# Optimization experiments

Hardware: AMD Instinct MI355X
Metric: run time of the kernel (lower is better)

## Reference

```python
import jax, jax.numpy as jnp
import numpy as np

SEQ, D_IN, D_OUT = 4096, 1024, 1024

def setup_inputs() -> dict:
    key = jax.random.key(0)
    k1, k2, k3, k4 = jax.random.split(key, 4)
    x = jax.random.normal(k1, (SEQ, D_IN), dtype=jnp.float32)
    # torch Linear weights have shape [d_out, d_in]; y = x @ W.T
    Wq = jax.random.normal(k2, (D_OUT, D_IN), dtype=jnp.float32) * (1.0 / np.sqrt(D_IN))
    Wk = jax.random.normal(k3, (D_OUT, D_IN), dtype=jnp.float32) * (1.0 / np.sqrt(D_IN))
    Wv = jax.random.normal(k4, (D_OUT, D_IN), dtype=jnp.float32) * (1.0 / np.sqrt(D_IN))
    return {"x": x, "Wq": Wq, "Wk": Wk, "Wv": Wv}

def reference(x, Wq, Wk, Wv):
    # q,k,v: [seq, d_out]
    q = x @ Wq.T
    k = x @ Wk.T
    v = x @ Wv.T
    scale = 1.0 / jnp.sqrt(jnp.asarray(k.shape[-1], dtype=x.dtype))
    scores = (q @ k.T) * scale            # [seq, seq]
    attn = jax.nn.softmax(scores, axis=1)  # softmax over key dim (dim=1)
    context = attn @ v                     # [seq, d_out]
    return context
```

## Files before the change

### kernel.cpp

```cpp
#include <hip/hip_runtime.h>

typedef __attribute__((ext_vector_type(4))) float f32x4;
typedef __attribute__((ext_vector_type(8))) short short8;
typedef _Float16 half8 __attribute__((ext_vector_type(8)));

__device__ __forceinline__ unsigned short f2h(float f) {
  _Float16 h = (_Float16)f;
  return __builtin_bit_cast(unsigned short, h);
}
__device__ __forceinline__ float h2f(unsigned short u) {
  return (float)__builtin_bit_cast(_Float16, u);
}

__global__ __launch_bounds__(256) void cast_kernel(const float* __restrict__ in,
                                                   unsigned short* __restrict__ out,
                                                   int n4) {
  int i = blockIdx.x * 256 + threadIdx.x;
  if (i >= n4) return;
  float4 v = ((const float4*)in)[i];
  ushort4 o;
  o.x = f2h(v.x); o.y = f2h(v.y); o.z = f2h(v.z); o.w = f2h(v.w);
  ((ushort4*)out)[i] = o;
}

__global__ __launch_bounds__(256) void cast3_kernel(const float* __restrict__ w0,
                                                    const float* __restrict__ w1,
                                                    const float* __restrict__ w2,
                                                    unsigned short* __restrict__ out) {
  const int b = blockIdx.x;
  const int seg = b >> 10;
  const float* src = (seg == 0) ? w0 : (seg == 1) ? w1 : w2;
  const int i = (b & 1023) * 256 + threadIdx.x;
  float4 v = ((const float4*)src)[i];
  ushort4 o;
  o.x = f2h(v.x); o.y = f2h(v.y); o.z = f2h(v.z); o.w = f2h(v.w);
  ((ushort4*)(out + (size_t)seg * 1048576))[i] = o;
}


#define PHASE(M0, STAGE, TAILWAIT)                                            \
  {                                                                           \
    _Pragma("unroll")                                                         \
    for (int mi = 0; mi < 2; ++mi) {                                          \
      _Pragma("unroll")                                                       \
      for (int ks = 0; ks < 2; ++ks) {                                        \
        const int row = (M0 + mi) * 16 + frow;                                \
        const int e = (row * 64 + ks * 32 + fk) ^ ((row & 7) << 3);           \
        af[mi][ks] = *(const half8*)(const void*)(Acur + e);                  \
      }                                                                       \
    }                                                                         \
    STAGE;                                                                    \
    __builtin_amdgcn_s_barrier();                                             \
    __builtin_amdgcn_s_setprio(1);                                            \
    _Pragma("unroll")                                                         \
    for (int ks = 0; ks < 2; ++ks)                                            \
      _Pragma("unroll")                                                       \
      for (int mi = 0; mi < 2; ++mi)                                          \
        _Pragma("unroll")                                                     \
        for (int n = 0; n < 4; ++n)                                           \
          acc[M0 + mi][n] = __builtin_amdgcn_mfma_f32_16x16x32_f16(           \
              af[mi][ks], bf[n][ks], acc[M0 + mi][n], 0, 0, 0);               \
    __builtin_amdgcn_s_setprio(0);                                            \
    TAILWAIT;                                                                 \
    __builtin_amdgcn_s_barrier();                                             \
  }

template <int MODE>
__global__ __launch_bounds__(512, 2) void gemm8(
    const unsigned short* __restrict__ A, int lda,
    const unsigned short* __restrict__ B, int ldb,
    int ksplit, float alpha,
    float* __restrict__ C0, int ldc0,
    unsigned short* __restrict__ H1, int ldh1,
    unsigned short* __restrict__ H2, int ldh2,
    unsigned short* __restrict__ H3, int ldh3,
    unsigned short* __restrict__ Cqk, int ldqk,
    unsigned short* __restrict__ CvT, int ldvt) {
  __shared__ __attribute__((aligned(16))) unsigned short lds[65536];

  const int t    = threadIdx.x;
  const int lane = t & 63;
  const int wave = t >> 6;
  const int wr   = wave >> 2;
  const int wc   = wave & 3;

  const int nx   = gridDim.x;
  const int nwg  = nx * gridDim.y;
  const int orig = blockIdx.y * nx + blockIdx.x;
  const int wg   = (orig & 7) * (nwg >> 3) + (orig >> 3);
  const int bm   = (wg / nx) * 256;
  const int bn   = (wg % nx) * 256;

  const int kbeg = blockIdx.z * ksplit;
  const int NT   = ksplit >> 6;

  const unsigned short* gA = A + (size_t)bm * lda;
  const unsigned short* gB = B + (size_t)bn * ldb;

  auto stage = [&](const unsigned short* gbase, int ld, int k0, unsigned short* dst) {
#pragma unroll
    for (int j = 0; j < 2; ++j) {
      const int de = t * 8 + j * 4096;
      const int se = de ^ (((de >> 6) & 7) << 3);
      __builtin_amdgcn_global_load_lds(
          (const __attribute__((address_space(1))) void*)(gbase + (size_t)(se >> 6) * ld + k0 + (se & 63)),
          (__attribute__((address_space(3))) void*)(dst + de),
          16, 0, 0);
    }
  };

  f32x4 acc[8][4];
#pragma unroll
  for (int i = 0; i < 8; ++i)
#pragma unroll
    for (int j = 0; j < 4; ++j)
      acc[i][j] = (f32x4){0.f, 0.f, 0.f, 0.f};

  const int frow = lane & 15;
  const int fk   = (lane >> 4) * 8;

  stage(gA,                     lda, kbeg, lds);
  stage(gA + (size_t)128 * lda, lda, kbeg, lds + 8192);
  stage(gB,                     ldb, kbeg, lds + 16384);
  stage(gB + (size_t)128 * ldb, ldb, kbeg, lds + 24576);
  if (NT > 1) {
    stage(gB,                     ldb, kbeg + 64, lds + 32768 + 16384);
    stage(gB + (size_t)128 * ldb, ldb, kbeg + 64, lds + 32768 + 24576);
    asm volatile("s_waitcnt vmcnt(4)" ::: "memory");
  } else {
    asm volatile("s_waitcnt vmcnt(0)" ::: "memory");
  }
  __builtin_amdgcn_s_barrier();

  for (int u = 0; u < NT; ++u) {
    const int cur = u & 1, nxt = cur ^ 1;
    const unsigned short* Acur = lds + cur * 32768 + wr * 8192;
    const unsigned short* Bcur = lds + cur * 32768 + 16384 + (wc >> 1) * 8192;
    const int brow0 = (wc & 1) * 64;

    half8 bf[4][2];
    half8 af[2][2];

#pragma unroll
    for (int n = 0; n < 4; ++n)
#pragma unroll
      for (int ks = 0; ks < 2; ++ks) {
        const int row = brow0 + n * 16 + frow;
        const int e = (row * 64 + ks * 32 + fk) ^ ((row & 7) << 3);
        bf[n][ks] = *(const half8*)(const void*)(Bcur + e);
      }

    PHASE(0,
          if (u + 1 < NT) stage(gA, lda, kbeg + (u + 1) * 64, lds + nxt * 32768),
          );
    PHASE(2,
          if (u + 1 < NT) stage(gA + (size_t)128 * lda, lda, kbeg + (u + 1) * 64, lds + nxt * 32768 + 8192),
          );
    PHASE(4,
          if (u + 2 < NT) stage(gB, ldb, kbeg + (u + 2) * 64, lds + cur * 32768 + 16384),
          );
    PHASE(6,
          if (u + 2 < NT) stage(gB + (size_t)128 * ldb, ldb, kbeg + (u + 2) * 64, lds + cur * 32768 + 24576),
          if (u + 2 < NT) { asm volatile("s_waitcnt vmcnt(4)" ::: "memory"); }
          else            { asm volatile("s_waitcnt vmcnt(0)" ::: "memory"); } );
  }

#pragma unroll
  for (int m = 0; m < 8; ++m) {
#pragma unroll
    for (int n = 0; n < 4; ++n) {
      const int row0 = bm + wr * 128 + m * 16 + (lane >> 4) * 4;
      const int col  = bn + wc * 64 + n * 16 + (lane & 15);
      if constexpr (MODE == 0) {
        if (blockIdx.z == 0) {
#pragma unroll
          for (int j = 0; j < 4; ++j)
            C0[(size_t)(row0 + j) * ldc0 + col] = acc[m][n][j] * alpha;
        } else {
          unsigned short* H; int ldh;
          if      (blockIdx.z == 1) { H = H1; ldh = ldh1; }
          else if (blockIdx.z == 2) { H = H2; ldh = ldh2; }
          else                      { H = H3; ldh = ldh3; }
#pragma unroll
          for (int j = 0; j < 4; ++j)
            H[(size_t)(row0 + j) * ldh + col] = f2h(acc[m][n][j] * alpha);
        }
      } else if constexpr (MODE == 1) {
#pragma unroll
        for (int j = 0; j < 4; ++j)
          Cqk[(size_t)(row0 + j) * ldqk + col] = f2h(acc[m][n][j] * alpha);
      } else {
        if (bn < 2048) {
#pragma unroll
          for (int j = 0; j < 4; ++j)
            Cqk[(size_t)(row0 + j) * ldqk + col] = f2h(acc[m][n][j] * alpha);
        } else {
          ushort4 o;
          o.x = f2h(acc[m][n][0] * alpha);
          o.y = f2h(acc[m][n][1] * alpha);
          o.z = f2h(acc[m][n][2] * alpha);
          o.w = f2h(acc[m][n][3] * alpha);
          *(ushort4*)(CvT + (size_t)(col - 2048) * ldvt + row0) = o;
        }
      }
    }
  }
}

__global__ __launch_bounds__(256) void softmax_rows(unsigned short* __restrict__ S) {
  const int row  = blockIdx.x;
  const int t    = threadIdx.x;
  const int lane = t & 63;
  const int wave = t >> 6;

  unsigned short* base = S + (size_t)row * 8192;
  ushort4 v[4];
  float f[16];
  float m = -3.0e38f;
#pragma unroll
  for (int i = 0; i < 4; ++i) {
    v[i] = ((const ushort4*)(base + t * 16))[i];
    f[4 * i + 0] = h2f(v[i].x);
    f[4 * i + 1] = h2f(v[i].y);
    f[4 * i + 2] = h2f(v[i].z);
    f[4 * i + 3] = h2f(v[i].w);
    m = fmaxf(m, fmaxf(fmaxf(f[4 * i + 0], f[4 * i + 1]), fmaxf(f[4 * i + 2], f[4 * i + 3])));
  }
#pragma unroll
  for (int off = 1; off < 64; off <<= 1)
    m = fmaxf(m, __shfl_xor(m, off));

  __shared__ float red[4];
  if (lane == 0) red[wave] = m;
  __syncthreads();
  m = fmaxf(fmaxf(red[0], red[1]), fmaxf(red[2], red[3]));
  __syncthreads();

  float s = 0.f;
#pragma unroll
  for (int i = 0; i < 16; ++i) {
    f[i] = __expf(f[i] - m);
    s += f[i];
  }
#pragma unroll
  for (int off = 1; off < 64; off <<= 1)
    s += __shfl_xor(s, off);
  if (lane == 0) red[wave] = s;
  __syncthreads();
  s = red[0] + red[1] + red[2] + red[3];
  const float inv = 512.0f / s;

#pragma unroll
  for (int i = 0; i < 4; ++i) {
    ushort4 o;
    o.x = f2h(f[4 * i + 0] * inv);
    o.y = f2h(f[4 * i + 1] * inv);
    o.z = f2h(f[4 * i + 2] * inv);
    o.w = f2h(f[4 * i + 3] * inv);
    ((ushort4*)(base + t * 16))[i] = o;
  }
}

__global__ __launch_bounds__(256) void combine4(float* __restrict__ out,
                                                const unsigned short* __restrict__ p1,
                                                const unsigned short* __restrict__ p2,
                                                const unsigned short* __restrict__ p3) {
  const int r = blockIdx.x, c = threadIdx.x;
  float4 o = ((float4*)(out + (size_t)r * 1024))[c];
  ushort4 a = ((const ushort4*)(p1 + (size_t)r * 1024))[c];
  ushort4 b = ((const ushort4*)(p2 + (size_t)r * 8192))[c];
  ushort4 d = ((const ushort4*)(p3 + (size_t)r * 8192))[c];
  o.x += h2f(a.x) + h2f(b.x) + h2f(d.x);
  o.y += h2f(a.y) + h2f(b.y) + h2f(d.y);
  o.z += h2f(a.z) + h2f(b.z) + h2f(d.z);
  o.w += h2f(a.w) + h2f(b.w) + h2f(d.w);
  ((float4*)(out + (size_t)r * 1024))[c] = o;
}

extern "C" void kernel_launch(void* const* d_in, const int* in_sizes, int n_in,
                              void* d_out, int out_size, void* d_ws, size_t ws_size,
                              hipStream_t stream) {
  const float* x  = (const float*)d_in[0];
  const float* Wq = (const float*)d_in[1];
  const float* Wk = (const float*)d_in[2];
  const float* Wv = (const float*)d_in[3];

  char* ws = (char*)d_ws;
  unsigned short* Sh    = (unsigned short*)ws;
  unsigned short* Hp2   = (unsigned short*)(ws + 8192);
  unsigned short* Hp3   = (unsigned short*)(ws + 12288);
  unsigned short* QK    = (unsigned short*)(ws + 67108864);
  unsigned short* Hp1   = (unsigned short*)(ws + 67108864);
  unsigned short* vT    = (unsigned short*)(ws + 83886080);
  unsigned short* xb    = (unsigned short*)(ws + 92274688);
  unsigned short* Wcat  = (unsigned short*)(ws + 100663296);

  cast_kernel<<<4096, 256, 0, stream>>>(x, xb, 1048576);
  cast3_kernel<<<3072, 256, 0, stream>>>(Wq, Wk, Wv, Wcat);

  gemm8<2><<<dim3(12, 16, 1), 512, 0, stream>>>(
      xb, 1024, Wcat, 1024, 1024, 1.0f,
      nullptr, 0, nullptr, 0, nullptr, 0, nullptr, 0, QK, 2048, vT, 4096);

  gemm8<1><<<dim3(16, 16, 1), 512, 0, stream>>>(
      QK, 2048, QK + 1024, 2048, 1024, 0.03125f,
      nullptr, 0, nullptr, 0, nullptr, 0, nullptr, 0, Sh, 8192, nullptr, 0);

  softmax_rows<<<4096, 256, 0, stream>>>(Sh);

  gemm8<0><<<dim3(4, 16, 4), 512, 0, stream>>>(
      Sh, 8192, vT, 4096, 1024, 1.0f / 512.0f,
      (float*)d_out, 1024, Hp1, 1024, Hp2, 8192, Hp3, 8192, nullptr, 0, nullptr, 0);
  combine4<<<4096, 256, 0, stream>>>((float*)d_out, Hp1, Hp2, Hp3);
}
```

Before: 154.4 us.

## Shrink GEMM tile to 128x256, drop LDS double buffering, raise occupancy

Rewrites the GEMM kernel to use a 128x256 block tile with a single LDS buffer, a simple load-wait-compute loop, and half the accumulator registers. Launch bounds target 4 blocks per CU and the grids double in the M dimension. The V-transpose epilogue now goes through LDS to make coalesced 16-byte stores. This trades the software-pipelined prefetch for occupancy-based latency hiding, and risks exposed global load latency plus lower arithmetic intensity per tile.

```diff
diff --git a/kernel.cpp b/kernel.cpp
--- a/kernel.cpp
+++ b/kernel.cpp
@@ -37,36 +37,8 @@
   ((ushort4*)(out + (size_t)seg * 1048576))[i] = o;
 }
 
-
-#define PHASE(M0, STAGE, TAILWAIT)                                            \
-  {                                                                           \
-    _Pragma("unroll")                                                         \
-    for (int mi = 0; mi < 2; ++mi) {                                          \
-      _Pragma("unroll")                                                       \
-      for (int ks = 0; ks < 2; ++ks) {                                        \
-        const int row = (M0 + mi) * 16 + frow;                                \
-        const int e = (row * 64 + ks * 32 + fk) ^ ((row & 7) << 3);           \
-        af[mi][ks] = *(const half8*)(const void*)(Acur + e);                  \
-      }                                                                       \
-    }                                                                         \
-    STAGE;                                                                    \
-    __builtin_amdgcn_s_barrier();                                             \
-    __builtin_amdgcn_s_setprio(1);                                            \
-    _Pragma("unroll")                                                         \
-    for (int ks = 0; ks < 2; ++ks)                                            \
-      _Pragma("unroll")                                                       \
-      for (int mi = 0; mi < 2; ++mi)                                          \
-        _Pragma("unroll")                                                     \
-        for (int n = 0; n < 4; ++n)                                           \
-          acc[M0 + mi][n] = __builtin_amdgcn_mfma_f32_16x16x32_f16(           \
-              af[mi][ks], bf[n][ks], acc[M0 + mi][n], 0, 0, 0);               \
-    __builtin_amdgcn_s_setprio(0);                                            \
-    TAILWAIT;                                                                 \
-    __builtin_amdgcn_s_barrier();                                             \
-  }
-
 template <int MODE>
-__global__ __launch_bounds__(512, 2) void gemm8(
+__global__ __launch_bounds__(512, 4) void gemm8(
     const unsigned short* __restrict__ A, int lda,
     const unsigned short* __restrict__ B, int ldb,
     int ksplit, float alpha,
@@ -76,7 +48,7 @@
     unsigned short* __restrict__ H3, int ldh3,
     unsigned short* __restrict__ Cqk, int ldqk,
     unsigned short* __restrict__ CvT, int ldvt) {
-  __shared__ __attribute__((aligned(16))) unsigned short lds[65536];
+  __shared__ __attribute__((aligned(16))) unsigned short lds[24576];
 
   const int t    = threadIdx.x;
   const int lane = t & 63;
@@ -88,7 +60,7 @@
   const int nwg  = nx * gridDim.y;
   const int orig = blockIdx.y * nx + blockIdx.x;
   const int wg   = (orig & 7) * (nwg >> 3) + (orig >> 3);
-  const int bm   = (wg / nx) * 256;
+  const int bm   = (wg / nx) * 128;
   const int bn   = (wg % nx) * 256;
 
   const int kbeg = blockIdx.z * ksplit;
@@ -109,69 +81,60 @@
     }
   };
 
-  f32x4 acc[8][4];
-#pragma unroll
-  for (int i = 0; i < 8; ++i)
+  f32x4 acc[4][4];
+#pragma unroll
+  for (int i = 0; i < 4; ++i)
 #pragma unroll
     for (int j = 0; j < 4; ++j)
       acc[i][j] = (f32x4){0.f, 0.f, 0.f, 0.f};
 
-  const int frow = lane & 15;
-  const int fk   = (lane >> 4) * 8;
-
-  stage(gA,                     lda, kbeg, lds);
-  stage(gA + (size_t)128 * lda, lda, kbeg, lds + 8192);
-  stage(gB,                     ldb, kbeg, lds + 16384);
-  stage(gB + (size_t)128 * ldb, ldb, kbeg, lds + 24576);
-  if (NT > 1) {
-    stage(gB,                     ldb, kbeg + 64, lds + 32768 + 16384);
-    stage(gB + (size_t)128 * ldb, ldb, kbeg + 64, lds + 32768 + 24576);
-    asm volatile("s_waitcnt vmcnt(4)" ::: "memory");
-  } else {
+  const int frow  = lane & 15;
+  const int fk    = (lane >> 4) * 8;
+  const int brow0 = (wc & 1) * 64;
+
+  for (int u = 0; u < NT; ++u) {
+    const int k0 = kbeg + u * 64;
+    stage(gA,                     lda, k0, lds);
+    stage(gB,                     ldb, k0, lds + 8192);
+    stage(gB + (size_t)128 * ldb, ldb, k0, lds + 16384);
     asm volatile("s_waitcnt vmcnt(0)" ::: "memory");
-  }
-  __builtin_amdgcn_s_barrier();
-
-  for (int u = 0; u < NT; ++u) {
-    const int cur = u & 1, nxt = cur ^ 1;
-    const unsigned short* Acur = lds + cur * 32768 + wr * 8192;
-    const unsigned short* Bcur = lds + cur * 32768 + 16384 + (wc >> 1) * 8192;
-    const int brow0 = (wc & 1) * 64;
-
+    __builtin_amdgcn_s_barrier();
+
+    const unsigned short* Bb = lds + 8192 + (wc >> 1) * 8192;
     half8 bf[4][2];
-    half8 af[2][2];
-
 #pragma unroll
     for (int n = 0; n < 4; ++n)
 #pragma unroll
       for (int ks = 0; ks < 2; ++ks) {
         const int row = brow0 + n * 16 + frow;
         const int e = (row * 64 + ks * 32 + fk) ^ ((row & 7) << 3);
-        bf[n][ks] = *(const half8*)(const void*)(Bcur + e);
+        bf[n][ks] = *(const half8*)(const void*)(Bb + e);
       }
 
-    PHASE(0,
-          if (u + 1 < NT) stage(gA, lda, kbeg + (u + 1) * 64, lds + nxt * 32768),
-          );
-    PHASE(2,
-          if (u + 1 < NT) stage(gA + (size_t)128 * lda, lda, kbeg + (u + 1) * 64, lds + nxt * 32768 + 8192),
-          );
-    PHASE(4,
-          if (u + 2 < NT) stage(gB, ldb, kbeg + (u + 2) * 64, lds + cur * 32768 + 16384),
-          );
-    PHASE(6,
-          if (u + 2 < NT) stage(gB + (size_t)128 * ldb, ldb, kbeg + (u + 2) * 64, lds + cur * 32768 + 24576),
-          if (u + 2 < NT) { asm volatile("s_waitcnt vmcnt(4)" ::: "memory"); }
-          else            { asm volatile("s_waitcnt vmcnt(0)" ::: "memory"); } );
-  }
-
-#pragma unroll
-  for (int m = 0; m < 8; ++m) {
-#pragma unroll
-    for (int n = 0; n < 4; ++n) {
-      const int row0 = bm + wr * 128 + m * 16 + (lane >> 4) * 4;
-      const int col  = bn + wc * 64 + n * 16 + (lane & 15);
-      if constexpr (MODE == 0) {
+    __builtin_amdgcn_s_setprio(1);
+#pragma unroll
+    for (int m = 0; m < 4; ++m) {
+      const int row = wr * 64 + m * 16 + frow;
+      const half8 a0 = *(const half8*)(const void*)(lds + ((row * 64 + fk) ^ ((row & 7) << 3)));
+      const half8 a1 = *(const half8*)(const void*)(lds + ((row * 64 + 32 + fk) ^ ((row & 7) << 3)));
+#pragma unroll
+      for (int n = 0; n < 4; ++n)
+        acc[m][n] = __builtin_amdgcn_mfma_f32_16x16x32_f16(a0, bf[n][0], acc[m][n], 0, 0, 0);
+#pragma unroll
+      for (int n = 0; n < 4; ++n)
+        acc[m][n] = __builtin_amdgcn_mfma_f32_16x16x32_f16(a1, bf[n][1], acc[m][n], 0, 0, 0);
+    }
+    __builtin_amdgcn_s_setprio(0);
+    __builtin_amdgcn_s_barrier();
+  }
+
+  if constexpr (MODE == 0) {
+#pragma unroll
+    for (int m = 0; m < 4; ++m) {
+#pragma unroll
+      for (int n = 0; n < 4; ++n) {
+        const int row0 = bm + wr * 64 + m * 16 + (lane >> 4) * 4;
+        const int col  = bn + wc * 64 + n * 16 + (lane & 15);
         if (blockIdx.z == 0) {
 #pragma unroll
           for (int j = 0; j < 4; ++j)
@@ -185,23 +148,57 @@
           for (int j = 0; j < 4; ++j)
             H[(size_t)(row0 + j) * ldh + col] = f2h(acc[m][n][j] * alpha);
         }
-      } else if constexpr (MODE == 1) {
+      }
+    }
+  } else if constexpr (MODE == 1) {
+#pragma unroll
+    for (int m = 0; m < 4; ++m)
+#pragma unroll
+      for (int n = 0; n < 4; ++n) {
+        const int row0 = bm + wr * 64 + m * 16 + (lane >> 4) * 4;
+        const int col  = bn + wc * 64 + n * 16 + (lane & 15);
 #pragma unroll
         for (int j = 0; j < 4; ++j)
           Cqk[(size_t)(row0 + j) * ldqk + col] = f2h(acc[m][n][j] * alpha);
-      } else {
-        if (bn < 2048) {
+      }
+  } else {
+    if (bn < 2048) {
+#pragma unroll
+      for (int m = 0; m < 4; ++m)
+#pragma unroll
+        for (int n = 0; n < 4; ++n) {
+          const int row0 = bm + wr * 64 + m * 16 + (lane >> 4) * 4;
+          const int col  = bn + wc * 64 + n * 16 + (lane & 15);
 #pragma unroll
           for (int j = 0; j < 4; ++j)
             Cqk[(size_t)(row0 + j) * ldqk + col] = f2h(acc[m][n][j] * alpha);
-        } else {
-          ushort4 o;
-          o.x = f2h(acc[m][n][0] * alpha);
-          o.y = f2h(acc[m][n][1] * alpha);
-          o.z = f2h(acc[m][n][2] * alpha);
-          o.w = f2h(acc[m][n][3] * alpha);
-          *(ushort4*)(CvT + (size_t)(col - 2048) * ldvt + row0) = o;
         }
+    } else {
+#pragma unroll
+      for (int p = 0; p < 2; ++p) {
+        __syncthreads();
+        if ((wc >> 1) == p) {
+#pragma unroll
+          for (int m = 0; m < 4; ++m)
+#pragma unroll
+            for (int n = 0; n < 4; ++n) {
+              const int cl = (wc & 1) * 64 + n * 16 + (lane & 15);
+              const int r  = wr * 64 + m * 16 + (lane >> 4) * 4;
+              ushort4 o;
+              o.x = f2h(acc[m][n][0] * alpha);
+              o.y = f2h(acc[m][n][1] * alpha);
+              o.z = f2h(acc[m][n][2] * alpha);
+              o.w = f2h(acc[m][n][3] * alpha);
+              *(ushort4*)(lds + cl * 136 + r) = o;
+            }
+        }
+        __syncthreads();
+        const int cl = t >> 2, roff = (t & 3) * 32;
+        const unsigned short* src = lds + cl * 136 + roff;
+        unsigned short* dst = CvT + (size_t)(bn - 2048 + p * 128 + cl) * ldvt + bm + roff;
+#pragma unroll
+        for (int i = 0; i < 4; ++i)
+          *(short8*)(dst + i * 8) = *(const short8*)(src + i * 8);
       }
     }
   }
@@ -298,17 +295,17 @@
   cast_kernel<<<4096, 256, 0, stream>>>(x, xb, 1048576);
   cast3_kernel<<<3072, 256, 0, stream>>>(Wq, Wk, Wv, Wcat);
 
-  gemm8<2><<<dim3(12, 16, 1), 512, 0, stream>>>(
+  gemm8<2><<<dim3(12, 32, 1), 512, 0, stream>>>(
       xb, 1024, Wcat, 1024, 1024, 1.0f,
       nullptr, 0, nullptr, 0, nullptr, 0, nullptr, 0, QK, 2048, vT, 4096);
 
-  gemm8<1><<<dim3(16, 16, 1), 512, 0, stream>>>(
+  gemm8<1><<<dim3(16, 32, 1), 512, 0, stream>>>(
       QK, 2048, QK + 1024, 2048, 1024, 0.03125f,
       nullptr, 0, nullptr, 0, nullptr, 0, nullptr, 0, Sh, 8192, nullptr, 0);
 
   softmax_rows<<<4096, 256, 0, stream>>>(Sh);
 
-  gemm8<0><<<dim3(4, 16, 4), 512, 0, stream>>>(
+  gemm8<0><<<dim3(4, 32, 4), 512, 0, stream>>>(
       Sh, 8192, vT, 4096, 1024, 1.0f / 512.0f,
       (float*)d_out, 1024, Hp1, 1024, Hp2, 8192, Hp3, 8192, nullptr, 0, nullptr, 0);
   combine4<<<4096, 256, 0, stream>>>((float*)d_out, Hp1, Hp2, Hp3);
```

Result: no change. 152.9 us (-1.0%).
